# Kernel optimization log

Measured on AMD Instinct MI355X. Metric: run time of the kernel, lower is better.

The kernel has to match this reference:

```python
import jax, jax.numpy as jnp
import numpy as np

D_FFN = 1536
SEQ = 512
N_SLICE = 0
D24 = D_FFN // 24  # 64
EPS = 1e-5

def gelu(x):
    return jax.nn.gelu(x, approximate=False)

def setup_inputs() -> dict:
    key = jax.random.key(0)
    ks = jax.random.split(key, 10)
    B = 32
    x = jax.random.normal(ks[0], (B, SEQ, D_FFN), dtype=jnp.float32)
    # LayerNorm params
    ln_g = jnp.ones((D_FFN,), jnp.float32)
    ln_b = jnp.zeros((D_FFN,), jnp.float32)
    # spatial_cls: Linear(D24->10), Conv1d(SEQ->1,k=1), Linear(10->1)
    w1 = jax.random.normal(ks[1], (D24, 10), jnp.float32) * 0.1
    b1 = jnp.zeros((10,), jnp.float32)
    wc = jax.random.normal(ks[2], (SEQ,), jnp.float32) * 0.04
    bc = jnp.zeros((), jnp.float32)
    w2 = jax.random.normal(ks[3], (10, 1), jnp.float32) * 0.3
    b2 = jnp.zeros((1,), jnp.float32)
    # expert conv1d (kernel size 1) weights: [S_out, S_in]
    Wi = jax.random.normal(ks[4], (SEQ, SEQ), jnp.float32) * 0.04
    bi = -jnp.ones((SEQ,), jnp.float32)   # nn.init.constant_(bias, -1.0)
    Wii = jax.random.normal(ks[5], (SEQ, SEQ), jnp.float32) * 0.04
    bii = jnp.ones((SEQ,), jnp.float32)   # nn.init.constant_(bias, 1.0)
    return {"x": x, "ln_g": ln_g, "ln_b": ln_b, "w1": w1, "b1": b1,
            "wc": wc, "bc": bc, "w2": w2, "b2": b2,
            "Wi": Wi, "bi": bi, "Wii": Wii, "bii": bii}

def reference(x, ln_g, ln_b, w1, b1, wc, bc, w2, b2, Wi, bi, Wii, bii):
    residual = x
    # LayerNorm over d_ffn
    mu = jnp.mean(x, axis=-1, keepdims=True)
    var = jnp.mean((x - mu) ** 2, axis=-1, keepdims=True)
    xn = (x - mu) * jax.lax.rsqrt(var + EPS) * ln_g + ln_b  # [B,S,D]
    # CLS gate: slice -> Linear -> GELU -> Conv1d(S->1,k1) -> GELU -> Linear -> Sigmoid
    c = xn[:, :, N_SLICE * D24:(N_SLICE + 1) * D24]          # [B,S,64]
    h = gelu(jnp.einsum('bsd,dk->bsk', c, w1) + b1)          # [B,S,10]
    h = gelu(jnp.einsum('bsk,s->bk', h, wc) + bc)            # [B,10]
    g = jax.nn.sigmoid(h @ w2 + b2)                          # [B,1]
    idx = jnp.round(jnp.squeeze(g, -1))                      # [B], 0. or 1.
    # hard-routed per-sample conv1d experts (k=1 => [S,S] matmul over seq dim)
    out_i = jnp.einsum('st,btd->bsd', Wi, xn) + bi[:, None]
    out_ii = jnp.einsum('st,btd->bsd', Wii, xn) + bii[:, None]
    out = jnp.where(idx[:, None, None] == 0, out_i, out_ii)
    return gelu(out + residual)
```

## Files before the change

kernel.cpp:

```cpp
#include <hip/hip_runtime.h>
#include <hip/hip_bf16.h>
#include <cstddef>

#define B 32
#define S 512
#define D 1536
#define D24 64
#define EPS 1e-5f

typedef float float4v __attribute__((ext_vector_type(4)));
typedef short short8 __attribute__((ext_vector_type(8)));

__device__ __forceinline__ float gelu_exact(float v) {
    return 0.5f * v * (1.0f + erff(v * 0.70710678118654752440f));
}

__device__ __forceinline__ float gelu_fast(float v) {
    float u = v * v;
    float z = v * __builtin_fmaf(0.07135481627f, u, 1.5957691216f);
    return v / (1.0f + __expf(-z));
}

__device__ __forceinline__ unsigned short f2bf(float f) {
    union { float f; unsigned u; } x; x.f = f;
    unsigned r = x.u + 0x7fffu + ((x.u >> 16) & 1u);
    return (unsigned short)(r >> 16);
}

__global__ __launch_bounds__(256) void ln_kernel(const float* __restrict__ x,
                                                 const float* __restrict__ ln_g,
                                                 const float* __restrict__ ln_b,
                                                 unsigned short* __restrict__ xnT,
                                                 float* __restrict__ cbufT) {
    const int b  = blockIdx.y;
    const int t0 = blockIdx.x * 64;
    const int tid  = threadIdx.x;
    const int lane = tid & 63;
    const int w    = tid >> 6;

    __shared__ float tile[64][65];
    __shared__ float lmu[64], lrs[64];

    for (int r = 0; r < 16; r++) {
        int row = w * 16 + r;
        const float4* xr = (const float4*)(x + ((size_t)(b * S + t0 + row)) * D);
        float s1 = 0.f, s2 = 0.f;
#pragma unroll
        for (int j = 0; j < 6; j++) {
            float4 v = xr[lane + j * 64];
            s1 += v.x + v.y + v.z + v.w;
            s2 += v.x * v.x + v.y * v.y + v.z * v.z + v.w * v.w;
        }
#pragma unroll
        for (int off = 32; off > 0; off >>= 1) {
            s1 += __shfl_down(s1, off, 64);
            s2 += __shfl_down(s2, off, 64);
        }
        if (lane == 0) {
            float mu  = s1 * (1.0f / D);
            float var = s2 * (1.0f / D) - mu * mu;
            lmu[row] = mu;
            lrs[row] = rsqrtf(var + EPS);
        }
    }
    __syncthreads();

    const int dq = (tid & 15) * 4;
    const int rg = tid >> 4;
    const int t8  = (tid & 7) * 8;
    const int dr0 = tid >> 3;

    for (int dt = 0; dt < 24; dt++) {
        const int d0 = dt * 64;
        float4 g4 = *(const float4*)(ln_g + d0 + dq);
        float4 b4 = *(const float4*)(ln_b + d0 + dq);
#pragma unroll
        for (int p = 0; p < 4; p++) {
            int row  = rg + p * 16;
            float mu   = lmu[row];
            float rstd = lrs[row];
            float4 v = *(const float4*)(x + ((size_t)(b * S + t0 + row)) * D + d0 + dq);
            tile[row][dq + 0] = (v.x - mu) * rstd * g4.x + b4.x;
            tile[row][dq + 1] = (v.y - mu) * rstd * g4.y + b4.y;
            tile[row][dq + 2] = (v.z - mu) * rstd * g4.z + b4.z;
            tile[row][dq + 3] = (v.w - mu) * rstd * g4.w + b4.w;
        }
        __syncthreads();
#pragma unroll
        for (int p = 0; p < 2; p++) {
            int drow = dr0 + p * 32;
            float fv[8];
            unsigned short bv[8];
#pragma unroll
            for (int j = 0; j < 8; j++) { fv[j] = tile[t8 + j][drow]; bv[j] = f2bf(fv[j]); }
            *(short8*)(xnT + ((size_t)b * D + d0 + drow) * S + t0 + t8) = *(const short8*)bv;
            if (dt == 0) {
                float* cp = cbufT + ((size_t)b * D24 + drow) * S + t0 + t8;
                *(float4*)(cp + 0) = (float4){fv[0], fv[1], fv[2], fv[3]};
                *(float4*)(cp + 4) = (float4){fv[4], fv[5], fv[6], fv[7]};
            }
        }
        __syncthreads();
    }
}

__global__ __launch_bounds__(256) void convw_kernel(const float* __restrict__ Wi,
                                                    const float* __restrict__ Wii,
                                                    unsigned short* __restrict__ wbf) {
    int i = (blockIdx.x * 256 + threadIdx.x) * 4;
    const float* src = (i < S * S) ? (Wi + i) : (Wii + i - S * S);
    float4 v = *(const float4*)src;
    unsigned short o[4] = {f2bf(v.x), f2bf(v.y), f2bf(v.z), f2bf(v.w)};
    *(uint2*)(wbf + i) = *(const uint2*)o;
}

__global__ __launch_bounds__(256) void gateA_kernel(const float* __restrict__ cbufT,
                                                    const float* __restrict__ w1,
                                                    const float* __restrict__ b1,
                                                    const float* __restrict__ wc,
                                                    float* __restrict__ partial) {
    const int b  = blockIdx.x >> 1;
    const int sb = blockIdx.x & 1;
    const int tid = threadIdx.x;
    const int s = sb * 256 + tid;
    __shared__ float w1s[D24 * 10];
    __shared__ float wsum[4][10];
    for (int i = tid; i < D24 * 10; i += 256) w1s[i] = w1[i];
    __syncthreads();

    float acc[10];
#pragma unroll
    for (int k = 0; k < 10; k++) acc[k] = b1[k];
    const float* cb = cbufT + (size_t)b * D24 * S + s;
#pragma unroll 8
    for (int i = 0; i < D24; i++) {
        float v = cb[(size_t)i * S];
#pragma unroll
        for (int k = 0; k < 10; k++) acc[k] += v * w1s[i * 10 + k];
    }
    float wcs = wc[s];
#pragma unroll
    for (int k = 0; k < 10; k++) {
        float t = gelu_exact(acc[k]) * wcs;
#pragma unroll
        for (int off = 32; off > 0; off >>= 1) t += __shfl_down(t, off, 64);
        if ((tid & 63) == 0) wsum[tid >> 6][k] = t;
    }
    __syncthreads();
    if (tid < 10)
        partial[blockIdx.x * 10 + tid] =
            wsum[0][tid] + wsum[1][tid] + wsum[2][tid] + wsum[3][tid];
}

__global__ __launch_bounds__(64) void gateB_kernel(const float* __restrict__ partial,
                                                   const float* __restrict__ bc,
                                                   const float* __restrict__ w2,
                                                   const float* __restrict__ b2,
                                                   int* __restrict__ sel) {
    int b = threadIdx.x;
    if (b < B) {
        float logit = b2[0];
        float bc0 = bc[0];
#pragma unroll
        for (int k = 0; k < 10; k++) {
            float ssum = partial[(b * 2) * 10 + k] + partial[(b * 2 + 1) * 10 + k];
            logit += gelu_exact(ssum + bc0) * w2[k];
        }
        sel[b] = (logit >= 0.f) ? 1 : 0;
    }
}

__global__ __launch_bounds__(256, 2) void gemm_kernel(const unsigned short* __restrict__ xnT,
                                                      const unsigned short* __restrict__ wbf,
                                                      const int* __restrict__ sel,
                                                      const float* __restrict__ bi,
                                                      const float* __restrict__ bii,
                                                      const float* __restrict__ x,
                                                      float* __restrict__ out) {
    const int b  = blockIdx.z;
    const int s0 = blockIdx.y * 128;
    const int d0 = blockIdx.x * 128;
    const int tid  = threadIdx.x;
    const int lane = tid & 63;
    const int wid  = tid >> 6;
    const int wm = (wid & 1) * 64;
    const int wn = (wid >> 1) * 64;
    const int q   = lane >> 4;
    const int r16 = lane & 15;

    const int ssel = sel[b];
    const unsigned short* W = wbf + (size_t)ssel * S * S;
    const float* bias = ssel ? bii : bi;
    const unsigned short* Xb = xnT + (size_t)b * D * S;

    __shared__ __align__(16) unsigned short As[2][128 * 64];
    __shared__ __align__(16) unsigned short Bs[2][128 * 64];

    auto stage = [&](int k0, int bf) {
#pragma unroll
        for (int i = 0; i < 4; i++) {
            int L = i * 256 + tid;
            int row = L >> 3;
            int sc  = L & 7;
            int c16 = sc ^ (row & 7);
            const unsigned short* gaA = W  + (size_t)(s0 + row) * S + k0 + c16 * 8;
            const unsigned short* gaB = Xb + (size_t)(d0 + row) * S + k0 + c16 * 8;
            unsigned short* laA = As[bf] + (size_t)(i * 256 + wid * 64) * 8;
            unsigned short* laB = Bs[bf] + (size_t)(i * 256 + wid * 64) * 8;
            __builtin_amdgcn_global_load_lds(
                (const __attribute__((address_space(1))) void*)gaA,
                (__attribute__((address_space(3))) void*)laA, 16, 0, 0);
            __builtin_amdgcn_global_load_lds(
                (const __attribute__((address_space(1))) void*)gaB,
                (__attribute__((address_space(3))) void*)laB, 16, 0, 0);
        }
    };

    float4v acc[4][4];
#pragma unroll
    for (int mi = 0; mi < 4; mi++)
#pragma unroll
        for (int ni = 0; ni < 4; ni++) acc[mi][ni] = (float4v){0.f, 0.f, 0.f, 0.f};

    stage(0, 0);
    __syncthreads();

    for (int it = 0; it < 8; it++) {
        const int cur = it & 1;
        if (it < 7) stage((it + 1) * 64, cur ^ 1);

        const unsigned short* Ac = As[cur];
        const unsigned short* Bc = Bs[cur];
#pragma unroll
        for (int h = 0; h < 2; h++) {
            short8 af[4], bfr[4];
#pragma unroll
            for (int mi = 0; mi < 4; mi++) {
                int row = wm + mi * 16 + r16;
                af[mi] = *(const short8*)(Ac + row * 64 + (((h << 2) + q) ^ (r16 & 7)) * 8);
            }
#pragma unroll
            for (int ni = 0; ni < 4; ni++) {
                int row = wn + ni * 16 + r16;
                bfr[ni] = *(const short8*)(Bc + row * 64 + (((h << 2) + q) ^ (r16 & 7)) * 8);
            }
#pragma unroll
            for (int mi = 0; mi < 4; mi++)
#pragma unroll
                for (int ni = 0; ni < 4; ni++)
                    acc[mi][ni] = __builtin_amdgcn_mfma_f32_16x16x32_bf16(
                        af[mi], bfr[ni], acc[mi][ni], 0, 0, 0);
        }
        __syncthreads();
    }

#pragma unroll
    for (int mi = 0; mi < 4; mi++) {
        int srow = s0 + wm + mi * 16 + q * 4;
#pragma unroll
        for (int ni = 0; ni < 4; ni++) {
            int d = d0 + wn + ni * 16 + r16;
#pragma unroll
            for (int r = 0; r < 4; r++) {
                int ss = srow + r;
                size_t gi = ((size_t)b * S + ss) * D + d;
                float v = acc[mi][ni][r] + bias[ss] + x[gi];
                out[gi] = gelu_fast(v);
            }
        }
    }
}

extern "C" void kernel_launch(void* const* d_in, const int* in_sizes, int n_in,
                              void* d_out, int out_size, void* d_ws, size_t ws_size,
                              hipStream_t stream) {
    const float* x    = (const float*)d_in[0];
    const float* ln_g = (const float*)d_in[1];
    const float* ln_b = (const float*)d_in[2];
    const float* w1   = (const float*)d_in[3];
    const float* b1   = (const float*)d_in[4];
    const float* wc   = (const float*)d_in[5];
    const float* bc   = (const float*)d_in[6];
    const float* w2   = (const float*)d_in[7];
    const float* b2   = (const float*)d_in[8];
    const float* Wi   = (const float*)d_in[9];
    const float* bi   = (const float*)d_in[10];
    const float* Wii  = (const float*)d_in[11];
    const float* bii  = (const float*)d_in[12];
    float* out = (float*)d_out;

    char* ws = (char*)d_ws;
    const size_t XNT_BYTES   = (size_t)B * D * S * 2;
    const size_t C_BYTES     = (size_t)B * D24 * S * 4;
    const size_t WBF_BYTES   = (size_t)2 * S * S * 2;
    const size_t PART_BYTES  = (size_t)B * 2 * 10 * 4;
    unsigned short* xnT   = (unsigned short*)ws;
    float*          cbufT = (float*)(ws + XNT_BYTES);
    unsigned short* wbf   = (unsigned short*)(ws + XNT_BYTES + C_BYTES);
    float*          part  = (float*)(ws + XNT_BYTES + C_BYTES + WBF_BYTES);
    int*            sel   = (int*)(ws + XNT_BYTES + C_BYTES + WBF_BYTES + PART_BYTES);

    ln_kernel<<<dim3(S / 64, B), 256, 0, stream>>>(x, ln_g, ln_b, xnT, cbufT);
    convw_kernel<<<(2 * S * S) / 1024, 256, 0, stream>>>(Wi, Wii, wbf);
    gateA_kernel<<<B * 2, 256, 0, stream>>>(cbufT, w1, b1, wc, part);
    gateB_kernel<<<1, 64, 0, stream>>>(part, bc, w2, b2, sel);
    gemm_kernel<<<dim3(D / 128, S / 128, B), 256, 0, stream>>>(xnT, wbf, sel, bi, bii, x, out);
}
```

Baseline: 288.0 us.

## Fuse LN, weight convert and gate into one prep kernel; blocked xnT layout

Merges the LayerNorm/transpose, weight bf16 conversion and gate stage-A kernels into a single prep kernel. The gate partials are accumulated with LDS and global atomics, and the final gate logit is computed inside the GEMM kernel. This removes three launches and the fp32 cbufT round trip. Each LN block now handles 16 rows instead of 64, and xnT is stored in a 16-token-blocked layout so each store is contiguous, which changes the GEMM B-operand addressing. The cost is a memset launch and atomics whose summation order is nondeterministic, plus more blocks that each do less work.

```diff
diff --git a/kernel.cpp b/kernel.cpp
--- a/kernel.cpp
+++ b/kernel.cpp
@@ -27,23 +27,46 @@
     return (unsigned short)(r >> 16);
 }
 
-__global__ __launch_bounds__(256) void ln_kernel(const float* __restrict__ x,
-                                                 const float* __restrict__ ln_g,
-                                                 const float* __restrict__ ln_b,
-                                                 unsigned short* __restrict__ xnT,
-                                                 float* __restrict__ cbufT) {
-    const int b  = blockIdx.y;
-    const int t0 = blockIdx.x * 64;
-    const int tid  = threadIdx.x;
+__global__ __launch_bounds__(256) void prep_kernel(const float* __restrict__ x,
+                                                   const float* __restrict__ ln_g,
+                                                   const float* __restrict__ ln_b,
+                                                   const float* __restrict__ w1,
+                                                   const float* __restrict__ b1,
+                                                   const float* __restrict__ wc,
+                                                   const float* __restrict__ Wi,
+                                                   const float* __restrict__ Wii,
+                                                   unsigned short* __restrict__ xnT,
+                                                   unsigned short* __restrict__ wbf,
+                                                   float* __restrict__ part) {
+    const int blk = blockIdx.x;
+    const int tid = threadIdx.x;
+
+    if (blk >= 1024) {
+        int i = ((blk - 1024) * 256 + tid) * 4;
+        const float* src = (i < S * S) ? (Wi + i) : (Wii + i - S * S);
+        float4 v = *(const float4*)src;
+        unsigned short o[4] = {f2bf(v.x), f2bf(v.y), f2bf(v.z), f2bf(v.w)};
+        *(uint2*)(wbf + i) = *(const uint2*)o;
+        return;
+    }
+
+    const int b    = blk >> 5;
+    const int tile = blk & 31;
+    const int t0   = tile * 16;
     const int lane = tid & 63;
     const int w    = tid >> 6;
 
-    __shared__ float tile[64][65];
-    __shared__ float lmu[64], lrs[64];
-
-    for (int r = 0; r < 16; r++) {
-        int row = w * 16 + r;
-        const float4* xr = (const float4*)(x + ((size_t)(b * S + t0 + row)) * D);
+    __shared__ float tl[16][65];
+    __shared__ float lmu[16], lrs[16];
+    __shared__ float w1s[D24 * 10];
+    __shared__ float lds_part[10];
+
+    for (int i = tid; i < D24 * 10; i += 256) w1s[i] = w1[i];
+    if (tid < 10) lds_part[tid] = 0.f;
+
+    for (int r = 0; r < 4; r++) {
+        int row = w * 4 + r;
+        const float4* xr = (const float4*)(x + (size_t)(b * S + t0 + row) * D);
         float s1 = 0.f, s2 = 0.f;
 #pragma unroll
         for (int j = 0; j < 6; j++) {
@@ -65,114 +88,49 @@
     }
     __syncthreads();
 
-    const int dq = (tid & 15) * 4;
-    const int rg = tid >> 4;
-    const int t8  = (tid & 7) * 8;
-    const int dr0 = tid >> 3;
+    const int rrow = tid >> 4;
+    const int dq   = (tid & 15) * 4;
+    const int drow = tid >> 1;
+    const int t8   = (tid & 1) * 8;
 
     for (int dt = 0; dt < 24; dt++) {
         const int d0 = dt * 64;
-        float4 g4 = *(const float4*)(ln_g + d0 + dq);
-        float4 b4 = *(const float4*)(ln_b + d0 + dq);
-#pragma unroll
-        for (int p = 0; p < 4; p++) {
-            int row  = rg + p * 16;
-            float mu   = lmu[row];
-            float rstd = lrs[row];
-            float4 v = *(const float4*)(x + ((size_t)(b * S + t0 + row)) * D + d0 + dq);
-            tile[row][dq + 0] = (v.x - mu) * rstd * g4.x + b4.x;
-            tile[row][dq + 1] = (v.y - mu) * rstd * g4.y + b4.y;
-            tile[row][dq + 2] = (v.z - mu) * rstd * g4.z + b4.z;
-            tile[row][dq + 3] = (v.w - mu) * rstd * g4.w + b4.w;
+        {
+            float4 g4 = *(const float4*)(ln_g + d0 + dq);
+            float4 b4 = *(const float4*)(ln_b + d0 + dq);
+            float mu = lmu[rrow], rstd = lrs[rrow];
+            float4 v = *(const float4*)(x + (size_t)(b * S + t0 + rrow) * D + d0 + dq);
+            tl[rrow][dq + 0] = (v.x - mu) * rstd * g4.x + b4.x;
+            tl[rrow][dq + 1] = (v.y - mu) * rstd * g4.y + b4.y;
+            tl[rrow][dq + 2] = (v.z - mu) * rstd * g4.z + b4.z;
+            tl[rrow][dq + 3] = (v.w - mu) * rstd * g4.w + b4.w;
         }
         __syncthreads();
-#pragma unroll
-        for (int p = 0; p < 2; p++) {
-            int drow = dr0 + p * 32;
-            float fv[8];
+        if (tid < 128) {
             unsigned short bv[8];
 #pragma unroll
-            for (int j = 0; j < 8; j++) { fv[j] = tile[t8 + j][drow]; bv[j] = f2bf(fv[j]); }
-            *(short8*)(xnT + ((size_t)b * D + d0 + drow) * S + t0 + t8) = *(const short8*)bv;
-            if (dt == 0) {
-                float* cp = cbufT + ((size_t)b * D24 + drow) * S + t0 + t8;
-                *(float4*)(cp + 0) = (float4){fv[0], fv[1], fv[2], fv[3]};
-                *(float4*)(cp + 4) = (float4){fv[4], fv[5], fv[6], fv[7]};
-            }
+            for (int j = 0; j < 8; j++) bv[j] = f2bf(tl[t8 + j][drow]);
+            *(short8*)(xnT + (((size_t)(b * 32 + tile)) * D + d0 + drow) * 16 + t8) =
+                *(const short8*)bv;
+        }
+        if (dt == 0 && tid < 160) {
+            int s_l = tid / 10, k = tid - s_l * 10;
+            float d = b1[k];
+#pragma unroll
+            for (int i = 0; i < D24; i++) d += tl[s_l][i] * w1s[i * 10 + k];
+            atomicAdd(&lds_part[k], gelu_exact(d) * wc[t0 + s_l]);
         }
         __syncthreads();
-    }
-}
-
-__global__ __launch_bounds__(256) void convw_kernel(const float* __restrict__ Wi,
-                                                    const float* __restrict__ Wii,
-                                                    unsigned short* __restrict__ wbf) {
-    int i = (blockIdx.x * 256 + threadIdx.x) * 4;
-    const float* src = (i < S * S) ? (Wi + i) : (Wii + i - S * S);
-    float4 v = *(const float4*)src;
-    unsigned short o[4] = {f2bf(v.x), f2bf(v.y), f2bf(v.z), f2bf(v.w)};
-    *(uint2*)(wbf + i) = *(const uint2*)o;
-}
-
-__global__ __launch_bounds__(256) void gateA_kernel(const float* __restrict__ cbufT,
-                                                    const float* __restrict__ w1,
-                                                    const float* __restrict__ b1,
-                                                    const float* __restrict__ wc,
-                                                    float* __restrict__ partial) {
-    const int b  = blockIdx.x >> 1;
-    const int sb = blockIdx.x & 1;
-    const int tid = threadIdx.x;
-    const int s = sb * 256 + tid;
-    __shared__ float w1s[D24 * 10];
-    __shared__ float wsum[4][10];
-    for (int i = tid; i < D24 * 10; i += 256) w1s[i] = w1[i];
-    __syncthreads();
-
-    float acc[10];
-#pragma unroll
-    for (int k = 0; k < 10; k++) acc[k] = b1[k];
-    const float* cb = cbufT + (size_t)b * D24 * S + s;
-#pragma unroll 8
-    for (int i = 0; i < D24; i++) {
-        float v = cb[(size_t)i * S];
-#pragma unroll
-        for (int k = 0; k < 10; k++) acc[k] += v * w1s[i * 10 + k];
-    }
-    float wcs = wc[s];
-#pragma unroll
-    for (int k = 0; k < 10; k++) {
-        float t = gelu_exact(acc[k]) * wcs;
-#pragma unroll
-        for (int off = 32; off > 0; off >>= 1) t += __shfl_down(t, off, 64);
-        if ((tid & 63) == 0) wsum[tid >> 6][k] = t;
-    }
-    __syncthreads();
-    if (tid < 10)
-        partial[blockIdx.x * 10 + tid] =
-            wsum[0][tid] + wsum[1][tid] + wsum[2][tid] + wsum[3][tid];
-}
-
-__global__ __launch_bounds__(64) void gateB_kernel(const float* __restrict__ partial,
-                                                   const float* __restrict__ bc,
-                                                   const float* __restrict__ w2,
-                                                   const float* __restrict__ b2,
-                                                   int* __restrict__ sel) {
-    int b = threadIdx.x;
-    if (b < B) {
-        float logit = b2[0];
-        float bc0 = bc[0];
-#pragma unroll
-        for (int k = 0; k < 10; k++) {
-            float ssum = partial[(b * 2) * 10 + k] + partial[(b * 2 + 1) * 10 + k];
-            logit += gelu_exact(ssum + bc0) * w2[k];
-        }
-        sel[b] = (logit >= 0.f) ? 1 : 0;
+        if (dt == 0 && tid < 10) atomicAdd(part + b * 10 + tid, lds_part[tid]);
     }
 }
 
 __global__ __launch_bounds__(256, 2) void gemm_kernel(const unsigned short* __restrict__ xnT,
                                                       const unsigned short* __restrict__ wbf,
-                                                      const int* __restrict__ sel,
+                                                      const float* __restrict__ part,
+                                                      const float* __restrict__ bc,
+                                                      const float* __restrict__ w2,
+                                                      const float* __restrict__ b2,
                                                       const float* __restrict__ bi,
                                                       const float* __restrict__ bii,
                                                       const float* __restrict__ x,
@@ -188,7 +146,14 @@
     const int q   = lane >> 4;
     const int r16 = lane & 15;
 
-    const int ssel = sel[b];
+    float logit = b2[0];
+    {
+        float bc0 = bc[0];
+        const float* pb = part + b * 10;
+#pragma unroll
+        for (int k = 0; k < 10; k++) logit += gelu_exact(pb[k] + bc0) * w2[k];
+    }
+    const int ssel = (logit >= 0.f) ? 1 : 0;
     const unsigned short* W = wbf + (size_t)ssel * S * S;
     const float* bias = ssel ? bii : bi;
     const unsigned short* Xb = xnT + (size_t)b * D * S;
@@ -203,8 +168,10 @@
             int row = L >> 3;
             int sc  = L & 7;
             int c16 = sc ^ (row & 7);
-            const unsigned short* gaA = W  + (size_t)(s0 + row) * S + k0 + c16 * 8;
-            const unsigned short* gaB = Xb + (size_t)(d0 + row) * S + k0 + c16 * 8;
+            int t_abs = k0 + c16 * 8;
+            const unsigned short* gaA = W + (size_t)(s0 + row) * S + t_abs;
+            const unsigned short* gaB =
+                Xb + ((size_t)(t_abs >> 4) * D + (d0 + row)) * 16 + (t_abs & 15);
             unsigned short* laA = As[bf] + (size_t)(i * 256 + wid * 64) * 8;
             unsigned short* laB = Bs[bf] + (size_t)(i * 256 + wid * 64) * 8;
             __builtin_amdgcn_global_load_lds(
@@ -290,19 +257,15 @@
     float* out = (float*)d_out;
 
     char* ws = (char*)d_ws;
-    const size_t XNT_BYTES   = (size_t)B * D * S * 2;
-    const size_t C_BYTES     = (size_t)B * D24 * S * 4;
-    const size_t WBF_BYTES   = (size_t)2 * S * S * 2;
-    const size_t PART_BYTES  = (size_t)B * 2 * 10 * 4;
-    unsigned short* xnT   = (unsigned short*)ws;
-    float*          cbufT = (float*)(ws + XNT_BYTES);
-    unsigned short* wbf   = (unsigned short*)(ws + XNT_BYTES + C_BYTES);
-    float*          part  = (float*)(ws + XNT_BYTES + C_BYTES + WBF_BYTES);
-    int*            sel   = (int*)(ws + XNT_BYTES + C_BYTES + WBF_BYTES + PART_BYTES);
-
-    ln_kernel<<<dim3(S / 64, B), 256, 0, stream>>>(x, ln_g, ln_b, xnT, cbufT);
-    convw_kernel<<<(2 * S * S) / 1024, 256, 0, stream>>>(Wi, Wii, wbf);
-    gateA_kernel<<<B * 2, 256, 0, stream>>>(cbufT, w1, b1, wc, part);
-    gateB_kernel<<<1, 64, 0, stream>>>(part, bc, w2, b2, sel);
-    gemm_kernel<<<dim3(D / 128, S / 128, B), 256, 0, stream>>>(xnT, wbf, sel, bi, bii, x, out);
-}
+    const size_t XNT_BYTES = (size_t)B * D * S * 2;
+    const size_t WBF_BYTES = (size_t)2 * S * S * 2;
+    unsigned short* xnT  = (unsigned short*)ws;
+    unsigned short* wbf  = (unsigned short*)(ws + XNT_BYTES);
+    float*          part = (float*)(ws + XNT_BYTES + WBF_BYTES);
+
+    hipMemsetAsync(part, 0, (size_t)B * 10 * sizeof(float), stream);
+    prep_kernel<<<1536, 256, 0, stream>>>(x, ln_g, ln_b, w1, b1, wc, Wi, Wii,
+                                          xnT, wbf, part);
+    gemm_kernel<<<dim3(D / 128, S / 128, B), 256, 0, stream>>>(
+        xnT, wbf, part, bc, w2, b2, bi, bii, x, out);
+}
```

After: 268.3 us. 1.07x faster.
